# Optimization experiments

Measured on AMD Instinct MI355X. Metric: run time of the kernel, lower is better.

Reference implementation:

```python
import jax, jax.numpy as jnp
import numpy as np
from jax import lax

N, E, DIN, D, L, H, T, NE = 20000, 240000, 768, 256, 3, 4, 9, 8  # nodes, edges, input_dim, gnn_dim, layers, heads, tags, n_etype
DH = D // H
BN_EPS = 1e-5

def _bn(x, g, b):
    # eval-mode BatchNorm1d with running stats (mean=0, var=1)
    return x * (g / np.sqrt(1.0 + BN_EPS)) + b

def _gelu(x):
    return jax.nn.gelu(x, approximate=False)

def setup_inputs():
    key = jax.random.key(0)
    ks = iter(jax.random.split(key, 48))
    nrm = lambda shape: jax.random.normal(next(ks), shape, jnp.float32) * 0.02
    return {
        "node_emb": jax.random.normal(next(ks), (N, DIN), jnp.float32),
        "edge_index": jax.random.randint(next(ks), (2, E), 0, N),
        "edge_type": jax.random.randint(next(ks), (E,), 0, NE),
        "tag_gt": jax.random.randint(next(ks), (N,), 0, T),
        "W_lm2gnn": nrm((DIN, D)), "b_lm2gnn": jnp.zeros((D,)),
        "We1": nrm((L, NE + 1, D)), "be1": jnp.zeros((L, D)),
        "g1": jnp.ones((L, D)), "bb1": jnp.zeros((L, D)),
        "We2": nrm((L, D, D)), "be2": jnp.zeros((L, D)),
        "Wq": nrm((L, D, D)), "bq": jnp.zeros((L, D)),
        "Wk": nrm((L, 2 * D, D)), "bk": jnp.zeros((L, D)),
        "Wm": nrm((L, 2 * D, D)), "bm": jnp.zeros((L, D)),
        "Wp1": nrm((L, D, D)), "bp1": jnp.zeros((L, D)),
        "g2": jnp.ones((L, D)), "bb2": jnp.zeros((L, D)),
        "Wp2": nrm((L, D, D)), "bp2": jnp.zeros((L, D)),
        "Wo": nrm((D, D)), "bo": jnp.zeros((D,)),
        "Wc": nrm((D, D)), "bc": jnp.zeros((D,)),
        "Wt": nrm((D, T)), "bt": jnp.zeros((T,)),
        "crf_start": nrm((T,)), "crf_end": nrm((T,)), "crf_trans": nrm((T, T)),
    }

def _emissions(node_emb, edge_index, edge_type, W_lm2gnn, b_lm2gnn, We1, be1, g1, bb1,
               We2, be2, Wq, bq, Wk, bk, Wm, bm, Wp1, bp1, g2, bb2, Wp2, bp2,
               Wo, bo, Wc, bc, Wt, bt):
    H0 = _gelu(node_emb @ W_lm2gnn + b_lm2gnn)
    loop = jnp.arange(N)
    src = jnp.concatenate([edge_index[0], loop])          # (Etot,)
    dst = jnp.concatenate([edge_index[1], loop])
    # one-hot edge types + self-loop type NE
    ev = jnp.concatenate([jax.nn.one_hot(edge_type, NE + 1, dtype=jnp.float32),
                          jnp.zeros((N, NE + 1), jnp.float32).at[:, NE].set(1.0)], axis=0)
    deg = jax.ops.segment_sum(jnp.ones_like(src, jnp.float32), src, N)[src]  # src out-degree per edge
    X = H0
    for l in range(L):
        e = _bn(ev @ We1[l] + be1[l], g1[l], bb1[l])
        e = jax.nn.relu(e) @ We2[l] + be2[l]              # edge embeddings (Etot, D)
        x_i, x_j = X[dst], X[src]                          # target, source gathers
        q = (x_j @ Wq[l] + bq[l]).reshape(-1, H, DH)
        k = (x_i @ Wk[l][:D] + e @ Wk[l][D:] + bk[l]).reshape(-1, H, DH)
        m = (x_j @ Wm[l][:D] + e @ Wm[l][D:] + bm[l]).reshape(-1, H, DH)
        s = (q * k).sum(-1) / np.sqrt(DH)                  # (Etot, H)
        smax = jax.ops.segment_max(s, src, N)[src]
        ex = jnp.exp(s - smax)
        den = jax.ops.segment_sum(ex, src, N)[src]
        alpha = ex / (den + 1e-16) * deg[:, None]          # segment softmax over src, degree-scaled
        out_e = (m * alpha[:, :, None]).reshape(-1, D)
        aggr = jax.ops.segment_sum(out_e, dst, N)          # scatter-add to targets
        Xl = _bn(aggr @ Wp1[l] + bp1[l], g2[l], bb2[l])
        X = _gelu(jax.nn.relu(Xl) @ Wp2[l] + bp2[l])       # mlp then activation (dropout = eval identity)
    hidden = _gelu((H0 @ Wo + bo) + (X @ Wc + bc))
    return hidden @ Wt + bt                                # (N, T)

def reference(node_emb, edge_index, edge_type, tag_gt, W_lm2gnn, b_lm2gnn, We1, be1, g1, bb1,
              We2, be2, Wq, bq, Wk, bk, Wm, bm, Wp1, bp1, g2, bb2, Wp2, bp2,
              Wo, bo, Wc, bc, Wt, bt, crf_start, crf_end, crf_trans):
    em = _emissions(node_emb, edge_index, edge_type, W_lm2gnn, b_lm2gnn, We1, be1, g1, bb1,
                    We2, be2, Wq, bq, Wk, bk, Wm, bm, Wp1, bp1, g2, bb2, Wp2, bp2,
                    Wo, bo, Wc, bc, Wt, bt)
    # CRF Viterbi decode (batch=1, full-length mask)
    def vstep(score, em_t):
        cand = score[:, None] + crf_trans                  # (T, T)
        return jnp.max(cand, axis=0) + em_t, jnp.argmax(cand, axis=0)
    last, bps = lax.scan(vstep, crf_start + em[0], em[1:])
    last_tag = jnp.argmax(last + crf_end)
    def back(t, bp_t):
        prev = bp_t[t]
        return prev, prev
    _, prevs = lax.scan(back, last_tag, bps, reverse=True)
    path = jnp.concatenate([prevs, last_tag[None]])
    return path[None, :]                                   # (1, N) best tag sequence
```

## Files before the change

### kernel.cpp

```cpp
#include <hip/hip_runtime.h>

#define NN 20000
#define EE 240000
#define ETOTAL 260000
#define DIN 768
#define DD 256
#define NT 9

typedef __attribute__((ext_vector_type(2))) float f32x2;

__device__ __forceinline__ float gelu_f(float x) {
  return 0.5f * x * (1.0f + erff(x * 0.70710678118654752440f));
}

#define VSTEP_CORE(EIN, SIN, SOUT)                                        \
  asm volatile(                                                           \
    "s_nop 2\n\t"                                                         \
    "v_readlane_b32 s84, %[sv], 0\n\t"                                    \
    "v_readlane_b32 s85, %[sv], 1\n\t"                                    \
    "v_readlane_b32 s86, %[sv], 2\n\t"                                    \
    "v_readlane_b32 s87, %[sv], 3\n\t"                                    \
    "v_readlane_b32 s88, %[sv], 4\n\t"                                    \
    "v_readlane_b32 s89, %[sv], 5\n\t"                                    \
    "v_readlane_b32 s90, %[sv], 6\n\t"                                    \
    "v_readlane_b32 s91, %[sv], 7\n\t"                                    \
    "v_readlane_b32 s92, %[sv], 8\n\t"                                    \
    "v_pk_add_f32 v[80:81], s[84:85], %[u01]\n\t"                         \
    "v_pk_add_f32 v[82:83], s[86:87], %[u23]\n\t"                         \
    "v_pk_add_f32 v[84:85], s[88:89], %[u45]\n\t"                         \
    "v_pk_add_f32 v[86:87], s[90:91], %[u67]\n\t"                         \
    "v_add_f32 v88, s92, %[u8]\n\t"                                       \
    "v_max3_f32 v80, v80, v81, v82\n\t"                                   \
    "v_max3_f32 v83, v83, v84, v85\n\t"                                   \
    "v_max3_f32 v86, v86, v87, v88\n\t"                                   \
    "v_max3_f32 v80, v80, v83, v86\n\t"                                   \
    "v_add_f32 %[out], v80, %[e]\n\t"                                     \
    : [out]"=v"(SOUT)                                                     \
    : [sv]"v"(SIN), [e]"v"(EIN),                                          \
      [u01]"v"(tc01), [u23]"v"(tc23), [u45]"v"(tc45), [u67]"v"(tc67),     \
      [u8]"v"(tcol8)                                                      \
    : "s84","s85","s86","s87","s88","s89","s90","s91","s92",              \
      "v80","v81","v82","v83","v84","v85","v86","v87","v88")

#define RUN8(E0, E1) do {                                                 \
  float s0, s1, s2, s3, s4, s5, s6, s7;                                   \
  VSTEP_CORE((E0).x, s, s0); VSTEP_CORE((E0).y, s0, s1);                  \
  VSTEP_CORE((E0).z, s1, s2); VSTEP_CORE((E0).w, s2, s3);                 \
  float4 stq0; stq0.x = s0; stq0.y = s1; stq0.z = s2; stq0.w = s3;        \
  *(float4*)svp = stq0;                                                   \
  VSTEP_CORE((E1).x, s3, s4); VSTEP_CORE((E1).y, s4, s5);                 \
  VSTEP_CORE((E1).z, s5, s6); VSTEP_CORE((E1).w, s6, s7);                 \
  float4 stq1; stq1.x = s4; stq1.y = s5; stq1.z = s6; stq1.w = s7;        \
  *(float4*)(svp + 256) = stq1;                                           \
  s = s7; svp += 512;                                                     \
} while (0)

__global__ __launch_bounds__(256) void gemm_k(
    const float* __restrict__ A, const float* __restrict__ B,
    const float* __restrict__ bias,
    const float* __restrict__ bng, const float* __restrict__ bnb,
    float* __restrict__ C, int M, int K, int N, int act)
{
  __shared__ float As[32][64];
  __shared__ float Bs[32][64];
  const int tid = threadIdx.x;
  const int tx = tid & 15, ty = tid >> 4;
  const int m0 = blockIdx.y * 64, n0 = blockIdx.x * 64;
  float acc[4][4];
#pragma unroll
  for (int i = 0; i < 4; ++i)
#pragma unroll
    for (int j = 0; j < 4; ++j) acc[i][j] = 0.f;

  for (int kk = 0; kk < K; kk += 32) {
#pragma unroll
    for (int L = tid; L < 512; L += 256) {
      int r = L >> 3, c4 = L & 7;
      int gm = m0 + r;
      float4 v = make_float4(0.f, 0.f, 0.f, 0.f);
      if (gm < M) v = *(const float4*)(A + (size_t)gm * K + kk + c4 * 4);
      As[c4 * 4 + 0][r] = v.x; As[c4 * 4 + 1][r] = v.y;
      As[c4 * 4 + 2][r] = v.z; As[c4 * 4 + 3][r] = v.w;
    }
#pragma unroll
    for (int L = tid; L < 512; L += 256) {
      int r = L >> 4, c4 = L & 15;
      *(float4*)&Bs[r][c4 * 4] = *(const float4*)(B + (size_t)(kk + r) * N + n0 + c4 * 4);
    }
    __syncthreads();
#pragma unroll
    for (int k = 0; k < 32; ++k) {
      float a[4], b[4];
      *(float4*)a = *(const float4*)&As[k][ty * 4];
      *(float4*)b = *(const float4*)&Bs[k][tx * 4];
#pragma unroll
      for (int i = 0; i < 4; ++i)
#pragma unroll
        for (int j = 0; j < 4; ++j) acc[i][j] += a[i] * b[j];
    }
    __syncthreads();
  }
  const float bnc = 0.99999500003749968752f;
#pragma unroll
  for (int i = 0; i < 4; ++i) {
    int gm = m0 + ty * 4 + i;
    if (gm >= M) continue;
    float o[4];
#pragma unroll
    for (int j = 0; j < 4; ++j) {
      int n = n0 + tx * 4 + j;
      float x = acc[i][j];
      if (bias) x += bias[n];
      if (act == 1) x = gelu_f(x);
      else if (act == 2) { x = x * (bng[n] * bnc) + bnb[n]; x = fmaxf(x, 0.f); }
      o[j] = x;
    }
    *(float4*)(C + (size_t)gm * N + n0 + tx * 4) = *(const float4*)o;
  }
}

__global__ __launch_bounds__(256) void gemm3_k(
    const float* __restrict__ A, const float* __restrict__ B0,
    const float* __restrict__ bias0, const float* __restrict__ B1,
    const float* __restrict__ B2, float* __restrict__ C0,
    float* __restrict__ C1, float* __restrict__ C2, int M)
{
  __shared__ float As[32][64];
  __shared__ float Bs[3][32][64];
  const int tid = threadIdx.x;
  const int tx = tid & 15, ty = tid >> 4;
  const int m0 = blockIdx.y * 64, n0 = blockIdx.x * 64;
  float acc0[4][4], acc1[4][4], acc2[4][4];
#pragma unroll
  for (int i = 0; i < 4; ++i)
#pragma unroll
    for (int j = 0; j < 4; ++j) { acc0[i][j] = 0.f; acc1[i][j] = 0.f; acc2[i][j] = 0.f; }

  for (int kk = 0; kk < DD; kk += 32) {
#pragma unroll
    for (int L = tid; L < 512; L += 256) {
      int r = L >> 3, c4 = L & 7;
      int gm = m0 + r;
      float4 v = make_float4(0.f, 0.f, 0.f, 0.f);
      if (gm < M) v = *(const float4*)(A + (size_t)gm * DD + kk + c4 * 4);
      As[c4 * 4 + 0][r] = v.x; As[c4 * 4 + 1][r] = v.y;
      As[c4 * 4 + 2][r] = v.z; As[c4 * 4 + 3][r] = v.w;
    }
#pragma unroll
    for (int L = tid; L < 1536; L += 256) {
      int which = L >> 9, r = (L >> 4) & 31, c4 = L & 15;
      const float* Bp = (which == 0) ? B0 : (which == 1) ? B1 : B2;
      *(float4*)&Bs[which][r][c4 * 4] =
          *(const float4*)(Bp + (size_t)(kk + r) * DD + n0 + c4 * 4);
    }
    __syncthreads();
#pragma unroll
    for (int k = 0; k < 32; ++k) {
      float a[4], b0[4], b1[4], b2[4];
      *(float4*)a = *(const float4*)&As[k][ty * 4];
      *(float4*)b0 = *(const float4*)&Bs[0][k][tx * 4];
      *(float4*)b1 = *(const float4*)&Bs[1][k][tx * 4];
      *(float4*)b2 = *(const float4*)&Bs[2][k][tx * 4];
#pragma unroll
      for (int i = 0; i < 4; ++i)
#pragma unroll
        for (int j = 0; j < 4; ++j) {
          acc0[i][j] += a[i] * b0[j];
          acc1[i][j] += a[i] * b1[j];
          acc2[i][j] += a[i] * b2[j];
        }
    }
    __syncthreads();
  }
#pragma unroll
  for (int i = 0; i < 4; ++i) {
    int gm = m0 + ty * 4 + i;
    if (gm >= M) continue;
    float o0[4], o1[4], o2[4];
#pragma unroll
    for (int j = 0; j < 4; ++j) {
      int n = n0 + tx * 4 + j;
      o0[j] = acc0[i][j] + bias0[n];
      o1[j] = acc1[i][j];
      o2[j] = acc2[i][j];
    }
    *(float4*)(C0 + (size_t)gm * DD + n0 + tx * 4) = *(const float4*)o0;
    *(float4*)(C1 + (size_t)gm * DD + n0 + tx * 4) = *(const float4*)o1;
    *(float4*)(C2 + (size_t)gm * DD + n0 + tx * 4) = *(const float4*)o2;
  }
}

__global__ __launch_bounds__(256) void gemm_cat_k(
    const float* __restrict__ A1, const float* __restrict__ B1,
    const float* __restrict__ bias1, const float* __restrict__ A2,
    const float* __restrict__ B2, const float* __restrict__ bias2,
    float* __restrict__ C, int M)
{
  __shared__ float As[32][64];
  __shared__ float Bs[32][64];
  const int tid = threadIdx.x;
  const int tx = tid & 15, ty = tid >> 4;
  const int m0 = blockIdx.y * 64, n0 = blockIdx.x * 64;
  float acc[4][4];
#pragma unroll
  for (int i = 0; i < 4; ++i)
#pragma unroll
    for (int j = 0; j < 4; ++j) acc[i][j] = 0.f;

  for (int kk = 0; kk < 2 * DD; kk += 32) {
    const float* Ap = (kk < DD) ? A1 : A2;
    const float* Bp = (kk < DD) ? B1 : B2;
    const int ko = kk & (DD - 1);
#pragma unroll
    for (int L = tid; L < 512; L += 256) {
      int r = L >> 3, c4 = L & 7;
      int gm = m0 + r;
      float4 v = make_float4(0.f, 0.f, 0.f, 0.f);
      if (gm < M) v = *(const float4*)(Ap + (size_t)gm * DD + ko + c4 * 4);
      As[c4 * 4 + 0][r] = v.x; As[c4 * 4 + 1][r] = v.y;
      As[c4 * 4 + 2][r] = v.z; As[c4 * 4 + 3][r] = v.w;
    }
#pragma unroll
    for (int L = tid; L < 512; L += 256) {
      int r = L >> 4, c4 = L & 15;
      *(float4*)&Bs[r][c4 * 4] = *(const float4*)(Bp + (size_t)(ko + r) * DD + n0 + c4 * 4);
    }
    __syncthreads();
#pragma unroll
    for (int k = 0; k < 32; ++k) {
      float a[4], b[4];
      *(float4*)a = *(const float4*)&As[k][ty * 4];
      *(float4*)b = *(const float4*)&Bs[k][tx * 4];
#pragma unroll
      for (int i = 0; i < 4; ++i)
#pragma unroll
        for (int j = 0; j < 4; ++j) acc[i][j] += a[i] * b[j];
    }
    __syncthreads();
  }
#pragma unroll
  for (int i = 0; i < 4; ++i) {
    int gm = m0 + ty * 4 + i;
    if (gm >= M) continue;
    float o[4];
#pragma unroll
    for (int j = 0; j < 4; ++j) {
      int n = n0 + tx * 4 + j;
      o[j] = gelu_f(acc[i][j] + bias1[n] + bias2[n]);
    }
    *(float4*)(C + (size_t)gm * DD + n0 + tx * 4) = *(const float4*)o;
  }
}

__global__ __launch_bounds__(256) void edge_tables_k(
    const float* __restrict__ We1l, const float* __restrict__ be1l,
    const float* __restrict__ g1l, const float* __restrict__ bb1l,
    const float* __restrict__ We2l, const float* __restrict__ be2l,
    const float* __restrict__ WkEl, const float* __restrict__ bkl,
    const float* __restrict__ WmEl, const float* __restrict__ bml,
    float* __restrict__ ketab, float* __restrict__ metab)
{
  __shared__ float r_s[DD];
  __shared__ float e_s[DD];
  const int t = blockIdx.x, d = threadIdx.x;
  const float bnc = 0.99999500003749968752f;
  float pre = We1l[t * DD + d] + be1l[d];
  float bnv = pre * (g1l[d] * bnc) + bb1l[d];
  r_s[d] = fmaxf(bnv, 0.f);
  __syncthreads();
  float acc = 0.f;
  for (int c = 0; c < DD; ++c) acc += r_s[c] * We2l[c * DD + d];
  e_s[d] = acc + be2l[d];
  __syncthreads();
  float ka = 0.f, ma = 0.f;
  for (int c = 0; c < DD; ++c) {
    float ec = e_s[c];
    ka += ec * WkEl[c * DD + d];
    ma += ec * WmEl[c * DD + d];
  }
  ketab[t * DD + d] = ka + bkl[d];
  metab[t * DD + d] = ma + bml[d];
}

__global__ void deg_k(const int* __restrict__ ei, int* __restrict__ cnt,
                      int* __restrict__ cnt_d)
{
  for (int e = blockIdx.x * blockDim.x + threadIdx.x; e < EE; e += gridDim.x * blockDim.x) {
    atomicAdd(&cnt[ei[e]], 1);
    atomicAdd(&cnt_d[ei[EE + e]], 1);
  }
}

__global__ __launch_bounds__(256) void scan_k(const int* __restrict__ c,
                                              int* __restrict__ offs)
{
  __shared__ int part[257];
  const int tid = threadIdx.x;
  const int CH = (NN + 255) / 256;
  int a = tid * CH, b = a + CH; if (b > NN) b = NN;
  int s = 0;
  for (int i = a; i < b; ++i) s += c[i];
  part[tid] = s;
  __syncthreads();
  if (tid == 0) {
    int r = 0;
    for (int i = 0; i < 256; ++i) { int v = part[i]; part[i] = r; r += v; }
    part[256] = r;
  }
  __syncthreads();
  int r = part[tid];
  for (int i = a; i < b; ++i) { offs[i] = r; r += c[i]; }
  if (tid == 255) offs[NN] = part[256];
}

__global__ void fill_k(const int* __restrict__ key, const int* __restrict__ offs,
                       int* __restrict__ fc, int* __restrict__ eix)
{
  for (int e = blockIdx.x * blockDim.x + threadIdx.x; e < EE; e += gridDim.x * blockDim.x) {
    int d = key[e];
    int p = offs[d] + atomicAdd(&fc[d], 1);
    eix[p] = e;
  }
}

__global__ __launch_bounds__(256) void score_k(
    const float* __restrict__ Q, const float* __restrict__ Kn,
    const float* __restrict__ ketab, const int* __restrict__ ei,
    const int* __restrict__ et, float* __restrict__ sbuf)
{
  __shared__ float ke_s[NT * DD];
  for (int i = threadIdx.x; i < NT * DD; i += 256) ke_s[i] = ketab[i];
  __syncthreads();
  const int lane = threadIdx.x & 63, wave = threadIdx.x >> 6;
  const float4* Q4 = (const float4*)Q;
  const float4* K4 = (const float4*)Kn;
  for (int e = blockIdx.x * 4 + wave; e < ETOTAL; e += gridDim.x * 4) {
    int src, dst, t;
    if (e < EE) { src = ei[e]; dst = ei[EE + e]; t = et[e]; }
    else { src = dst = e - EE; t = NT - 1; }
    float4 q = Q4[src * 64 + lane];
    float4 k = K4[dst * 64 + lane];
    float4 ke = *(const float4*)(ke_s + t * DD + lane * 4);
    float p = q.x * (k.x + ke.x) + q.y * (k.y + ke.y) +
              q.z * (k.z + ke.z) + q.w * (k.w + ke.w);
    p += __shfl_xor(p, 8); p += __shfl_xor(p, 4);
    p += __shfl_xor(p, 2); p += __shfl_xor(p, 1);
    if ((lane & 15) == 0) {
      int h = lane >> 4;
      sbuf[e * 4 + h] = p * 0.125f;
    }
  }
}

__global__ __launch_bounds__(256) void smx_k(
    const float* __restrict__ sbuf, const int* __restrict__ offs_s,
    const int* __restrict__ eix_s, float2* __restrict__ sd)
{
  const int lane = threadIdx.x & 63, wave = threadIdx.x >> 6;
  const int h = lane >> 4, sl = lane & 15;
  int src = blockIdx.x * 4 + wave;
  if (src >= NN) return;
  int o0 = offs_s[src], o1 = offs_s[src + 1];
  float sself = sbuf[(EE + src) * 4 + h];
  float mx = (sl == 0) ? sself : -__builtin_inff();
  for (int o = o0 + sl; o < o1; o += 16) {
    int e = eix_s[o];
    mx = fmaxf(mx, sbuf[e * 4 + h]);
  }
#pragma unroll
  for (int m = 8; m >= 1; m >>= 1) mx = fmaxf(mx, __shfl_xor(mx, m));
  float sum = (sl == 0) ? expf(sself - mx) : 0.f;
  for (int o = o0 + sl; o < o1; o += 16) {
    int e = eix_s[o];
    sum += expf(sbuf[e * 4 + h] - mx);
  }
#pragma unroll
  for (int m = 8; m >= 1; m >>= 1) sum += __shfl_xor(sum, m);
  if (sl == 0) sd[src * 4 + h] = make_float2(mx, sum);
}

__global__ __launch_bounds__(256) void aggr2_k(
    const float* __restrict__ Mn, const float* __restrict__ metab,
    const int* __restrict__ ei, const int* __restrict__ et,
    const float* __restrict__ sbuf, const float2* __restrict__ sd,
    const int* __restrict__ cnt, const int* __restrict__ offs,
    const int* __restrict__ eix, float* __restrict__ aggr)
{
  __shared__ float me_s[NT * DD];
  for (int i = threadIdx.x; i < NT * DD; i += 256) me_s[i] = metab[i];
  __syncthreads();
  const int lane = threadIdx.x & 63, wave = threadIdx.x >> 6;
  const int h = lane >> 4;
  const float4* M4 = (const float4*)Mn;
  int dst = blockIdx.x * 4 + wave;
  if (dst >= NN) return;
  float4 acc;
  {
    float2 sdv = sd[dst * 4 + h];
    float ex = expf(sbuf[(EE + dst) * 4 + h] - sdv.x);
    float alpha = ex / (sdv.y + 1e-16f) * (float)(cnt[dst] + 1);
    float4 m = M4[dst * 64 + lane];
    float4 me = *(const float4*)(me_s + (NT - 1) * DD + lane * 4);
    acc.x = (m.x + me.x) * alpha; acc.y = (m.y + me.y) * alpha;
    acc.z = (m.z + me.z) * alpha; acc.w = (m.w + me.w) * alpha;
  }
  int o1 = offs[dst + 1];
  for (int o = offs[dst]; o < o1; ++o) {
    int e = eix[o];
    int src = ei[e], t = et[e];
    float2 sdv = sd[src * 4 + h];
    float ex = expf(sbuf[e * 4 + h] - sdv.x);
    float alpha = ex / (sdv.y + 1e-16f) * (float)(cnt[src] + 1);
    float4 m = M4[src * 64 + lane];
    float4 me = *(const float4*)(me_s + t * DD + lane * 4);
    acc.x += (m.x + me.x) * alpha; acc.y += (m.y + me.y) * alpha;
    acc.z += (m.z + me.z) * alpha; acc.w += (m.w + me.w) * alpha;
  }
  ((float4*)aggr)[dst * 64 + lane] = acc;
}

__global__ __launch_bounds__(256) void emis_k(
    const float* __restrict__ hidden, const float* __restrict__ Wt,
    const float* __restrict__ bt, float* __restrict__ em)
{
  __shared__ float wt_s[DD * NT];
  for (int i = threadIdx.x; i < DD * NT; i += 256) wt_s[i] = Wt[i];
  __syncthreads();
  const int lane = threadIdx.x & 63, wave = threadIdx.x >> 6;
  const float4* H4 = (const float4*)hidden;
  for (int n = blockIdx.x * 4 + wave; n < NN; n += gridDim.x * 4) {
    float4 h = H4[n * 64 + lane];
    const float* w0 = wt_s + (lane * 4) * NT;
    float p[NT];
#pragma unroll
    for (int t = 0; t < NT; ++t)
      p[t] = h.x * w0[t] + h.y * w0[NT + t] + h.z * w0[2 * NT + t] + h.w * w0[3 * NT + t];
#pragma unroll
    for (int m = 32; m >= 1; m >>= 1)
#pragma unroll
      for (int t = 0; t < NT; ++t) p[t] += __shfl_xor(p[t], m);
    if (lane == 0) {
#pragma unroll
      for (int t = 0; t < NT; ++t) em[n * NT + t] = p[t] + bt[t];
    }
  }
}

__global__ __launch_bounds__(256) void viterbi_k(
    const float* __restrict__ em, const float* __restrict__ cstart,
    const float* __restrict__ cend, const float* __restrict__ ctrans,
    float* __restrict__ sv, int* __restrict__ outp)
{
  const int VCS = 512;
  const int ST = VCS + 12;
  const int NCH = (NN + VCS - 1) / VCS;
  __shared__ float embufT[2][NT][VCS + 12];
  __shared__ float trT[NT * 16];
  __shared__ float scf[NT];
  __shared__ unsigned char fmaps[256][NT];
  __shared__ unsigned char ends_s[256];
  __shared__ int last_s;
  const int tid = threadIdx.x, lane = tid & 63, wave = tid >> 6;
  const int jl = min(lane & 15, NT - 1);

  for (int i = tid; i < VCS * NT; i += 256) {
    int t = i / NT, j = i - t * NT;
    embufT[0][j][t] = em[i];
  }
  if (tid < NT * NT) trT[(tid % NT) * 16 + (tid / NT)] = ctrans[tid];
  __syncthreads();

  f32x2 tc01, tc23, tc45, tc67;
  float tcol8 = 0.f;
  float s = 0.f;
  if (wave == 0) {
    tc01[0] = ctrans[0 * NT + jl]; tc01[1] = ctrans[1 * NT + jl];
    tc23[0] = ctrans[2 * NT + jl]; tc23[1] = ctrans[3 * NT + jl];
    tc45[0] = ctrans[4 * NT + jl]; tc45[1] = ctrans[5 * NT + jl];
    tc67[0] = ctrans[6 * NT + jl]; tc67[1] = ctrans[7 * NT + jl];
    tcol8   = ctrans[8 * NT + jl];
    s = cstart[jl] + embufT[0][jl][0];
    sv[lane * 4] = s;
  }

  for (int c = 0; c < NCH; ++c) {
    if (wave > 0) {
      if (c + 1 < NCH) {
        int base = (c + 1) * VCS * NT;
        int n2 = VCS * NT;
        if (base + n2 > NN * NT) n2 = NN * NT - base;
        float* dstb = &embufT[(c + 1) & 1][0][0];
        for (int i = tid - 64; i < n2; i += 192) {
          int t = i / NT, j = i - t * NT;
          dstb[j * ST + t] = em[base + i];
        }
      }
    } else {
      const float* ebT = &embufT[c & 1][0][0] + (size_t)jl * ST;
      int tbeg = (c == 0) ? 1 : c * VCS;
      int tend = (c + 1) * VCS; if (tend > NN) tend = NN;
      int off = tbeg - c * VCS;
      int nsteps = tend - tbeg;
      int pre = (8 - (tbeg & 7)) & 7; if (pre > nsteps) pre = nsteps;
      for (int i = 0; i < pre; ++i) {
        int t = tbeg + i;
        float e0 = ebT[off + i];
        float so;
        VSTEP_CORE(e0, s, so);
        s = so;
        sv[((size_t)t >> 2) * 256 + lane * 4 + (t & 3)] = s;
      }
      int rem = nsteps - pre;
      int ngr = rem >> 3;
      int tof = off + pre;
      float* svp = sv + ((size_t)(tbeg + pre) >> 2) * 256 + lane * 4;
      if (ngr > 0) {
        float4 eA0 = *(const float4*)&ebT[tof];
        float4 eA1 = *(const float4*)&ebT[tof + 4];
        float4 eB0, eB1;
        int g = 0;
        while (g + 2 <= ngr) {
          eB0 = *(const float4*)&ebT[tof + (g + 1) * 8];
          eB1 = *(const float4*)&ebT[tof + (g + 1) * 8 + 4];
          RUN8(eA0, eA1);
          eA0 = *(const float4*)&ebT[tof + (g + 2) * 8];
          eA1 = *(const float4*)&ebT[tof + (g + 2) * 8 + 4];
          RUN8(eB0, eB1);
          g += 2;
        }
        if (g < ngr) RUN8(eA0, eA1);
      }
      for (int i = pre + (ngr << 3); i < nsteps; ++i) {
        int t = tbeg + i;
        float e0 = ebT[off + i];
        float so;
        VSTEP_CORE(e0, s, so);
        s = so;
        sv[((size_t)t >> 2) * 256 + lane * 4 + (t & 3)] = s;
      }
    }
    __syncthreads();
  }

  if (wave == 0 && lane < NT) scf[lane] = s + cend[lane];
  __syncthreads();
  if (tid == 0) {
    float bv = scf[0]; int bi = 0;
    for (int j = 1; j < NT; ++j) if (scf[j] > bv) { bv = scf[j]; bi = j; }
    last_s = bi;
  }
  __syncthreads();

  const int RL = 79;
  int a = 1 + tid * RL;
  int b = a + RL; if (b > NN) b = NN;
  bool active = (a < NN);
  if (active) {
    int x[NT];
#pragma unroll
    for (int j = 0; j < NT; ++j) x[j] = j;
    for (int t = b - 1; t >= a; --t) {
      const float* sp = sv + ((size_t)(t - 1) >> 2) * 256 + ((t - 1) & 3);
      float sr[NT];
#pragma unroll
      for (int i = 0; i < NT; ++i) sr[i] = sp[i * 4];
#pragma unroll
      for (int j = 0; j < NT; ++j) {
        const float* tcx = trT + x[j] * 16;
        float bv = sr[0] + tcx[0]; int bi = 0;
#pragma unroll
        for (int i = 1; i < NT; ++i) {
          float cv = sr[i] + tcx[i];
          if (cv > bv) { bv = cv; bi = i; }
        }
        x[j] = bi;
      }
    }
#pragma unroll
    for (int j = 0; j < NT; ++j) fmaps[tid][j] = (unsigned char)x[j];
  }
  __syncthreads();
  if (tid == 0) {
    int x = last_s;
    for (int k = 255; k >= 0; --k) {
      ends_s[k] = (unsigned char)x;
      int ak = 1 + k * RL;
      if (ak < NN) x = fmaps[k][x];
    }
  }
  __syncthreads();
  if (active) {
    int x = ends_s[tid];
    outp[b - 1] = x;
    for (int t = b - 1; t >= a; --t) {
      const float* sp = sv + ((size_t)(t - 1) >> 2) * 256 + ((t - 1) & 3);
      const float* tcx = trT + x * 16;
      float bv = sp[0] + tcx[0]; int bi = 0;
#pragma unroll
      for (int i = 1; i < NT; ++i) {
        float cv = sp[i * 4] + tcx[i];
        if (cv > bv) { bv = cv; bi = i; }
      }
      x = bi;
      outp[t - 1] = x;
    }
  }
}

extern "C" void kernel_launch(void* const* d_in, const int* in_sizes, int n_in,
                              void* d_out, int out_size, void* d_ws, size_t ws_size,
                              hipStream_t stream)
{
  const float* node_emb = (const float*)d_in[0];
  const int* edge_index = (const int*)d_in[1];
  const int* edge_type = (const int*)d_in[2];
  const float* W_lm2gnn = (const float*)d_in[4];
  const float* b_lm2gnn = (const float*)d_in[5];
  const float* We1 = (const float*)d_in[6];
  const float* be1 = (const float*)d_in[7];
  const float* g1 = (const float*)d_in[8];
  const float* bb1 = (const float*)d_in[9];
  const float* We2 = (const float*)d_in[10];
  const float* be2 = (const float*)d_in[11];
  const float* Wq = (const float*)d_in[12];
  const float* bq = (const float*)d_in[13];
  const float* Wk = (const float*)d_in[14];
  const float* bk = (const float*)d_in[15];
  const float* Wm = (const float*)d_in[16];
  const float* bm = (const float*)d_in[17];
  const float* Wp1 = (const float*)d_in[18];
  const float* bp1 = (const float*)d_in[19];
  const float* g2 = (const float*)d_in[20];
  const float* bb2 = (const float*)d_in[21];
  const float* Wp2 = (const float*)d_in[22];
  const float* bp2 = (const float*)d_in[23];
  const float* Wo = (const float*)d_in[24];
  const float* bo = (const float*)d_in[25];
  const float* Wc = (const float*)d_in[26];
  const float* bc = (const float*)d_in[27];
  const float* Wt = (const float*)d_in[28];
  const float* bt = (const float*)d_in[29];
  const float* cstart = (const float*)d_in[30];
  const float* cend = (const float*)d_in[31];
  const float* ctrans = (const float*)d_in[32];

  const size_t NB = (size_t)NN * DD * sizeof(float);
  char* w = (char*)d_ws;
  float* H0 = (float*)(w + 0 * NB);
  float* Xb = (float*)(w + 1 * NB);
  float* Qb = (float*)(w + 2 * NB);
  float* Kb = (float*)(w + 3 * NB);
  float* Mb = (float*)(w + 4 * NB);
  char* sm = w + 5 * NB;
  size_t smo = 0;
  auto alloc = [&](size_t bytes) { char* p = sm + smo; smo += (bytes + 255) & ~255ull; return p; };
  float* sbuf = (float*)alloc((size_t)ETOTAL * 4 * 4);
  int* cnt = (int*)alloc((size_t)NN * 4);
  int* cnt_d = (int*)alloc((size_t)NN * 4);
  int* offs = (int*)alloc((size_t)(NN + 1) * 4);
  int* fc = (int*)alloc((size_t)NN * 4);
  int* offs_s = (int*)alloc((size_t)(NN + 1) * 4);
  int* fc_s = (int*)alloc((size_t)NN * 4);
  int* eix = (int*)alloc((size_t)EE * 4);
  int* eix_s = (int*)alloc((size_t)EE * 4);
  float2* sd = (float2*)alloc((size_t)NN * 4 * 8);
  float* ketab = (float*)alloc((size_t)NT * DD * 4);
  float* metab = (float*)alloc((size_t)NT * DD * 4);
  float* em = (float*)alloc((size_t)NN * NT * 4);
  float* sv = (float*)alloc(((size_t)NN * 64 + 256) * 4);
  const size_t needed = 5 * NB + smo;
  if (ws_size < needed) return;

  dim3 gg(DD / 64, (NN + 63) / 64);

  hipMemsetAsync(cnt, 0, (size_t)((char*)eix - (char*)cnt), stream);
  deg_k<<<1024, 256, 0, stream>>>(edge_index, cnt, cnt_d);
  scan_k<<<1, 256, 0, stream>>>(cnt_d, offs);
  scan_k<<<1, 256, 0, stream>>>(cnt, offs_s);
  fill_k<<<1024, 256, 0, stream>>>(edge_index + EE, offs, fc, eix);
  fill_k<<<1024, 256, 0, stream>>>(edge_index, offs_s, fc_s, eix_s);

  gemm_k<<<gg, 256, 0, stream>>>(node_emb, W_lm2gnn, b_lm2gnn, nullptr,
                                 nullptr, H0, NN, DIN, DD, 1);

  const float* Xcur = H0;
  for (int l = 0; l < 3; ++l) {
    edge_tables_k<<<NT, 256, 0, stream>>>(
        We1 + (size_t)l * NT * DD, be1 + l * DD, g1 + l * DD, bb1 + l * DD,
        We2 + (size_t)l * DD * DD, be2 + l * DD,
        Wk + (size_t)l * 2 * DD * DD + DD * DD, bk + l * DD,
        Wm + (size_t)l * 2 * DD * DD + DD * DD, bm + l * DD, ketab, metab);

    gemm3_k<<<gg, 256, 0, stream>>>(Xcur, Wq + (size_t)l * DD * DD, bq + l * DD,
                                    Wk + (size_t)l * 2 * DD * DD,
                                    Wm + (size_t)l * 2 * DD * DD,
                                    Qb, Kb, Mb, NN);

    score_k<<<2048, 256, 0, stream>>>(Qb, Kb, ketab, edge_index, edge_type, sbuf);
    smx_k<<<(NN + 3) / 4, 256, 0, stream>>>(sbuf, offs_s, eix_s, sd);

    aggr2_k<<<(NN + 3) / 4, 256, 0, stream>>>(Mb, metab, edge_index, edge_type,
                                              sbuf, sd, cnt, offs, eix, Kb);

    gemm_k<<<gg, 256, 0, stream>>>(Kb, Wp1 + (size_t)l * DD * DD, bp1 + l * DD,
                                   g2 + l * DD, bb2 + l * DD, Qb, NN, DD, DD, 2);
    gemm_k<<<gg, 256, 0, stream>>>(Qb, Wp2 + (size_t)l * DD * DD, bp2 + l * DD,
                                   nullptr, nullptr, Xb, NN, DD, DD, 1);
    Xcur = Xb;
  }

  gemm_cat_k<<<gg, 256, 0, stream>>>(H0, Wo, bo, Xb, Wc, bc, Qb, NN);

  emis_k<<<1250, 256, 0, stream>>>(Qb, Wt, bt, em);
  viterbi_k<<<1, 256, 0, stream>>>(em, cstart, cend, ctrans, sv, (int*)d_out);
}
```

Measured before the change: 2.741 ms.

## Fuse edge scoring with online softmax per source and pre-pack CSR edge metadata

```diff
diff --git a/kernel.cpp b/kernel.cpp
--- a/kernel.cpp
+++ b/kernel.cpp
@@ -323,68 +323,70 @@
   }
 }
 
-__global__ __launch_bounds__(256) void score_k(
+__global__ void pack_k(const int* __restrict__ ei, const int* __restrict__ et,
+                       const int* __restrict__ eix, const int* __restrict__ eix_s,
+                       int2* __restrict__ srcte_d, int2* __restrict__ dstte_s)
+{
+  for (int o = blockIdx.x * blockDim.x + threadIdx.x; o < EE; o += gridDim.x * blockDim.x) {
+    int e = eix[o];
+    srcte_d[o] = make_int2(ei[e], (e << 4) | et[e]);
+    int e2 = eix_s[o];
+    dstte_s[o] = make_int2(ei[EE + e2], (e2 << 4) | et[e2]);
+  }
+}
+
+__global__ __launch_bounds__(256) void score2_k(
     const float* __restrict__ Q, const float* __restrict__ Kn,
-    const float* __restrict__ ketab, const int* __restrict__ ei,
-    const int* __restrict__ et, float* __restrict__ sbuf)
+    const float* __restrict__ ketab, const int* __restrict__ offs_s,
+    const int2* __restrict__ dstte_s, float* __restrict__ sbuf,
+    float2* __restrict__ sd)
 {
   __shared__ float ke_s[NT * DD];
   for (int i = threadIdx.x; i < NT * DD; i += 256) ke_s[i] = ketab[i];
   __syncthreads();
   const int lane = threadIdx.x & 63, wave = threadIdx.x >> 6;
+  const int h = lane >> 4, sl = lane & 15;
   const float4* Q4 = (const float4*)Q;
   const float4* K4 = (const float4*)Kn;
-  for (int e = blockIdx.x * 4 + wave; e < ETOTAL; e += gridDim.x * 4) {
-    int src, dst, t;
-    if (e < EE) { src = ei[e]; dst = ei[EE + e]; t = et[e]; }
-    else { src = dst = e - EE; t = NT - 1; }
-    float4 q = Q4[src * 64 + lane];
+  int src = blockIdx.x * 4 + wave;
+  if (src >= NN) return;
+  float4 q = Q4[src * 64 + lane];
+  float mx, sum;
+  {
+    float4 k = K4[src * 64 + lane];
+    float4 ke = *(const float4*)(ke_s + (NT - 1) * DD + lane * 4);
+    float p = q.x * (k.x + ke.x) + q.y * (k.y + ke.y) +
+              q.z * (k.z + ke.z) + q.w * (k.w + ke.w);
+    p += __shfl_xor(p, 8); p += __shfl_xor(p, 4);
+    p += __shfl_xor(p, 2); p += __shfl_xor(p, 1);
+    float se = p * 0.125f;
+    if (sl == 0) sbuf[(EE + src) * 4 + h] = se;
+    mx = se; sum = 1.0f;
+  }
+  int o1 = offs_s[src + 1];
+  for (int o = offs_s[src]; o < o1; ++o) {
+    int2 dt = dstte_s[o];
+    int dst = dt.x, e = dt.y >> 4, t = dt.y & 15;
     float4 k = K4[dst * 64 + lane];
     float4 ke = *(const float4*)(ke_s + t * DD + lane * 4);
     float p = q.x * (k.x + ke.x) + q.y * (k.y + ke.y) +
               q.z * (k.z + ke.z) + q.w * (k.w + ke.w);
     p += __shfl_xor(p, 8); p += __shfl_xor(p, 4);
     p += __shfl_xor(p, 2); p += __shfl_xor(p, 1);
-    if ((lane & 15) == 0) {
-      int h = lane >> 4;
-      sbuf[e * 4 + h] = p * 0.125f;
-    }
-  }
-}
-
-__global__ __launch_bounds__(256) void smx_k(
-    const float* __restrict__ sbuf, const int* __restrict__ offs_s,
-    const int* __restrict__ eix_s, float2* __restrict__ sd)
-{
-  const int lane = threadIdx.x & 63, wave = threadIdx.x >> 6;
-  const int h = lane >> 4, sl = lane & 15;
-  int src = blockIdx.x * 4 + wave;
-  if (src >= NN) return;
-  int o0 = offs_s[src], o1 = offs_s[src + 1];
-  float sself = sbuf[(EE + src) * 4 + h];
-  float mx = (sl == 0) ? sself : -__builtin_inff();
-  for (int o = o0 + sl; o < o1; o += 16) {
-    int e = eix_s[o];
-    mx = fmaxf(mx, sbuf[e * 4 + h]);
-  }
-#pragma unroll
-  for (int m = 8; m >= 1; m >>= 1) mx = fmaxf(mx, __shfl_xor(mx, m));
-  float sum = (sl == 0) ? expf(sself - mx) : 0.f;
-  for (int o = o0 + sl; o < o1; o += 16) {
-    int e = eix_s[o];
-    sum += expf(sbuf[e * 4 + h] - mx);
-  }
-#pragma unroll
-  for (int m = 8; m >= 1; m >>= 1) sum += __shfl_xor(sum, m);
+    float se = p * 0.125f;
+    if (sl == 0) sbuf[e * 4 + h] = se;
+    float nm = fmaxf(mx, se);
+    sum = sum * expf(mx - nm) + expf(se - nm);
+    mx = nm;
+  }
   if (sl == 0) sd[src * 4 + h] = make_float2(mx, sum);
 }
 
 __global__ __launch_bounds__(256) void aggr2_k(
     const float* __restrict__ Mn, const float* __restrict__ metab,
-    const int* __restrict__ ei, const int* __restrict__ et,
     const float* __restrict__ sbuf, const float2* __restrict__ sd,
     const int* __restrict__ cnt, const int* __restrict__ offs,
-    const int* __restrict__ eix, float* __restrict__ aggr)
+    const int2* __restrict__ srcte_d, float* __restrict__ aggr)
 {
   __shared__ float me_s[NT * DD];
   for (int i = threadIdx.x; i < NT * DD; i += 256) me_s[i] = metab[i];
@@ -406,8 +408,8 @@
   }
   int o1 = offs[dst + 1];
   for (int o = offs[dst]; o < o1; ++o) {
-    int e = eix[o];
-    int src = ei[e], t = et[e];
+    int2 st = srcte_d[o];
+    int src = st.x, e = st.y >> 4, t = st.y & 15;
     float2 sdv = sd[src * 4 + h];
     float ex = expf(sbuf[e * 4 + h] - sdv.x);
     float alpha = ex / (sdv.y + 1e-16f) * (float)(cnt[src] + 1);
@@ -663,6 +665,8 @@
   int* fc_s = (int*)alloc((size_t)NN * 4);
   int* eix = (int*)alloc((size_t)EE * 4);
   int* eix_s = (int*)alloc((size_t)EE * 4);
+  int2* srcte_d = (int2*)alloc((size_t)EE * 8);
+  int2* dstte_s = (int2*)alloc((size_t)EE * 8);
   float2* sd = (float2*)alloc((size_t)NN * 4 * 8);
   float* ketab = (float*)alloc((size_t)NT * DD * 4);
   float* metab = (float*)alloc((size_t)NT * DD * 4);
@@ -679,6 +683,8 @@
   scan_k<<<1, 256, 0, stream>>>(cnt, offs_s);
   fill_k<<<1024, 256, 0, stream>>>(edge_index + EE, offs, fc, eix);
   fill_k<<<1024, 256, 0, stream>>>(edge_index, offs_s, fc_s, eix_s);
+  pack_k<<<1024, 256, 0, stream>>>(edge_index, edge_type, eix, eix_s,
+                                   srcte_d, dstte_s);
 
   gemm_k<<<gg, 256, 0, stream>>>(node_emb, W_lm2gnn, b_lm2gnn, nullptr,
                                  nullptr, H0, NN, DIN, DD, 1);
@@ -696,11 +702,11 @@
                                     Wm + (size_t)l * 2 * DD * DD,
                                     Qb, Kb, Mb, NN);
 
-    score_k<<<2048, 256, 0, stream>>>(Qb, Kb, ketab, edge_index, edge_type, sbuf);
-    smx_k<<<(NN + 3) / 4, 256, 0, stream>>>(sbuf, offs_s, eix_s, sd);
-
-    aggr2_k<<<(NN + 3) / 4, 256, 0, stream>>>(Mb, metab, edge_index, edge_type,
-                                              sbuf, sd, cnt, offs, eix, Kb);
+    score2_k<<<(NN + 3) / 4, 256, 0, stream>>>(Qb, Kb, ketab, offs_s,
+                                               dstte_s, sbuf, sd);
+
+    aggr2_k<<<(NN + 3) / 4, 256, 0, stream>>>(Mb, metab, sbuf, sd, cnt,
+                                              offs, srcte_d, Kb);
 
     gemm_k<<<gg, 256, 0, stream>>>(Kb, Wp1 + (size_t)l * DD * DD, bp1 + l * DD,
                                    g2 + l * DD, bb2 + l * DD, Qb, NN, DD, DD, 2);
```

Measured after the change: 2.647 ms. 1.04x faster.
